# Kernel optimization log

Hardware: AMD Instinct MI355X
Metric: run time of the kernel (lower is better)

## Reference

```python
import jax, jax.numpy as jnp
import numpy as np

ENC_DIM = 512
B, T = 2048, 256
NUM_PARTS, PART_DIM, ATT_DIM, VOCAB = 64, 32, 128, 12


def _p(key, shape, scale=0.05):
    return jax.random.normal(key, shape, dtype=jnp.float32) * scale


def setup_inputs() -> dict:
    key = jax.random.key(0)
    ks = jax.random.split(key, 24)
    inp = {
        "img_features": jax.random.normal(ks[0], (B, 32, 8, 8), dtype=jnp.float32),
        "label": jax.random.normal(ks[1], (B, T, VOCAB), dtype=jnp.float32),
        # Attention params
        "Ww": _p(ks[2], (ATT_DIM, PART_DIM)), "Wb": _p(ks[3], (ATT_DIM,)),
        "Uw": _p(ks[4], (ATT_DIM, ENC_DIM)), "Ub": _p(ks[5], (ATT_DIM,)),
        "vw": _p(ks[6], (1, ATT_DIM)), "vb": _p(ks[7], (1,)),
        "betaw": _p(ks[8], (PART_DIM, ENC_DIM)), "betab": _p(ks[9], (PART_DIM,)),
        # init hidden params
        "ihw": _p(ks[10], (ENC_DIM, NUM_PARTS)), "ihb": _p(ks[11], (ENC_DIM,)),
        "icw": _p(ks[12], (ENC_DIM, NUM_PARTS)), "icb": _p(ks[13], (ENC_DIM,)),
        # LSTMCell params (PyTorch layout: [4*H, in] / [4*H, H])
        "W_ih": _p(ks[14], (4 * ENC_DIM, VOCAB + PART_DIM)),
        "W_hh": _p(ks[15], (4 * ENC_DIM, ENC_DIM)),
        "b_ih": _p(ks[16], (4 * ENC_DIM,)), "b_hh": _p(ks[17], (4 * ENC_DIM,)),
        # output fc
        "ow": _p(ks[18], (VOCAB, ENC_DIM)), "ob": _p(ks[19], (VOCAB,)),
    }
    return inp


def reference(img_features, label, Ww, Wb, Uw, Ub, vw, vb, betaw, betab,
              ihw, ihb, icw, icb, W_ih, W_hh, b_ih, b_hh, ow, ob):
    b = img_features.shape[0]
    feats = img_features.reshape(b, 32, -1)          # [B, 32, 64]
    parts = feats.transpose(0, 2, 1)                  # [B, 64, 32]
    # init hidden/cell from mean over channel dim (dim=1 in torch)
    avg = feats.mean(axis=1)                          # [B, 64]
    h0 = jnp.tanh(avg @ ihw.T + ihb)                  # [B, H]
    c0 = jnp.tanh(avg @ icw.T + icb)
    # W_s depends only on img features: hoist out of the loop (same math)
    Ws = parts @ Ww.T + Wb                            # [B, 64, 128]
    lab = label.transpose(1, 0, 2)                    # [T, B, 12]

    H = h0.shape[1]

    def step(carry, x_t):
        h, c = carry
        Uh = h @ Uw.T + Ub                            # [B, 128]
        att = jnp.tanh(Ws + Uh[:, None, :])           # [B, 64, 128]
        score = (att @ vw.T + vb)[..., 0]             # [B, 64]
        alpha = jax.nn.softmax(score, axis=1)
        ctx = jnp.einsum('bp,bpd->bd', alpha, parts)  # [B, 32]
        beta = jax.nn.sigmoid(h @ betaw.T + betab)
        ctx = ctx * beta
        inp = jnp.concatenate([x_t, ctx], axis=1)     # [B, 44]
        gates = inp @ W_ih.T + b_ih + h @ W_hh.T + b_hh
        i, f, g, o = jnp.split(gates, 4, axis=1)
        c2 = jax.nn.sigmoid(f) * c + jax.nn.sigmoid(i) * jnp.tanh(g)
        h2 = jax.nn.sigmoid(o) * jnp.tanh(c2)
        out = h2 @ ow.T + ob                          # [B, 12]
        return (h2, c2), (out, alpha)

    (_, _), (outs, alphas) = jax.lax.scan(step, (h0, c0), lab)
    output = jax.nn.log_softmax(outs, axis=-1).transpose(1, 0, 2)  # [B, T, 12]
    return output, alphas  # alphas: [T, B, 64] (stacked version of the list)
```

## Files before the change

kernel.cpp:

```cpp
#include <hip/hip_runtime.h>
#include <hip/hip_bf16.h>


typedef __attribute__((ext_vector_type(8))) short short8;
typedef __attribute__((ext_vector_type(4))) float floatx4;
typedef __attribute__((ext_vector_type(2))) unsigned int uint2v;

#define DEV static __device__ __forceinline__
#define C2LE 2.885390082f
#define LOG2E 1.4426950409f
#define LN2 0.6931471806f

DEV unsigned short f2bf(float f) {
    unsigned int u = __float_as_uint(f);
    unsigned int r = (u + 0x7FFFu + ((u >> 16) & 1u)) >> 16;
    return (unsigned short)r;
}
DEV float bf2f(unsigned short u) { return __uint_as_float(((unsigned int)u) << 16); }
DEV float rcp_f(float x) { float r; asm("v_rcp_f32 %0, %1" : "=v"(r) : "v"(x)); return r; }
DEV float tanh_f(float x) { return 1.f - 2.f * rcp_f(1.f + exp2f(x * C2LE)); }
DEV float sigm(float x) { return rcp_f(1.f + exp2f(-x * LOG2E)); }

DEV void ldg16_sc(short8* d, const unsigned short* p) {
    asm volatile("global_load_dwordx4 %0, %1, off sc0 sc1" : "=v"(*d) : "v"(p));
}
DEV void stg16_sc(unsigned short* p, short8 v) {
    asm volatile("global_store_dwordx4 %0, %1, off sc0 sc1" :: "v"(p), "v"(v) : "memory");
}
DEV void stg8_sc(unsigned short* p, uint2v v) {
    asm volatile("global_store_dwordx2 %0, %1, off sc0 sc1" :: "v"(p), "v"(v) : "memory");
}
DEV void st_flag(int* p, int v) {
    asm volatile("global_store_dword %0, %1, off sc0 sc1" :: "v"(p), "v"(v) : "memory");
}
DEV int ld_flag(const int* p) {
    int v;
    asm volatile("global_load_dword %0, %1, off sc0 sc1\n\ts_waitcnt vmcnt(0)"
                 : "=v"(v) : "v"(p) : "memory");
    return v;
}
DEV void waitv0() { asm volatile("s_waitcnt vmcnt(0)" ::: "memory"); }

#define OFF_XH     ((size_t)0)
#define OFF_C0     ((size_t)2359296)
#define OFF_PARTS  ((size_t)6553600)
#define OFF_WBIG   ((size_t)14942208)
#define OFF_WSMALL ((size_t)17301504)
#define OFF_WW2    ((size_t)17465344)
#define OFF_BIAS   ((size_t)17473536)
#define OFF_AVG    ((size_t)17481728)
#define OFF_FLAGS  ((size_t)18006016)

DEV void gbar(int* flags, int bk, int g4, int step) {
    waitv0();
    __syncthreads();
    if (threadIdx.x < 64) {
        int lane = threadIdx.x;
        if (lane == 0) st_flag(flags + bk * 32, step);
        for (;;) {
            int v = step;
            if (lane < 4) v = ld_flag(flags + (g4 + lane) * 32);
            if (__all(v >= step)) break;
            __builtin_amdgcn_s_sleep(1);
        }
    }
    __syncthreads();
}

__global__ void k_init(int* flags) {
    int i = blockIdx.x * 256 + threadIdx.x;
    if (i < 256 * 32) flags[i] = 0;
}

__global__ void k_avg(const float* __restrict__ img, float* __restrict__ avg) {
    int idx = blockIdx.x * 256 + threadIdx.x;
    int b = idx >> 6, p = idx & 63;
    const float* base = img + (size_t)b * 2048 + p;
    float s = 0.f;
#pragma unroll
    for (int k = 0; k < 32; ++k) s += base[k * 64];
    avg[idx] = s * (1.f / 32.f);
}

__global__ void k_prep(const float* __restrict__ Whh, const float* __restrict__ Wih,
                       const float* __restrict__ Uw, const float* __restrict__ betaw,
                       const float* __restrict__ Ww, const float* __restrict__ bih,
                       const float* __restrict__ bhh,
                       unsigned short* __restrict__ Wbig, unsigned short* __restrict__ Wsmall,
                       unsigned short* __restrict__ Ww2, float* __restrict__ bias_cat) {
    int p = blockIdx.x, tid = threadIdx.x;
    int g = p & 3, j = p >> 2, orig = g * 512 + j;
    for (int k = tid; k < 576; k += 256) {
        float v = 0.f;
        if (k < 512) v = Whh[(size_t)orig * 512 + k];
        else if (k < 556) v = Wih[(size_t)orig * 44 + (k - 512)];
        Wbig[(size_t)p * 576 + k] = f2bf(v);
    }
    if (p < 160) {
        for (int k = tid; k < 512; k += 256) {
            float v = (p < 128) ? Uw[(size_t)p * 512 + k] : betaw[(size_t)(p - 128) * 512 + k];
            Wsmall[(size_t)p * 512 + k] = f2bf(v);
        }
    }
    if (p < 128 && tid < 32) Ww2[p * 32 + tid] = f2bf(C2LE * Ww[p * 32 + tid]);
    if (tid == 0) bias_cat[orig] = bih[orig] + bhh[orig];
}

__global__ __launch_bounds__(512) void k_h0c0(const float* __restrict__ avg,
                                              const float* __restrict__ ihw, const float* __restrict__ ihb,
                                              const float* __restrict__ icw, const float* __restrict__ icb,
                                              unsigned short* __restrict__ xh, float* __restrict__ c0) {
    __shared__ float avg_s[8][64];
    int b0 = blockIdx.x * 8, tid = threadIdx.x;
    for (int i = tid; i < 8 * 64; i += 512) avg_s[i >> 6][i & 63] = avg[b0 * 64 + i];
    __syncthreads();
    int j = tid;
    float w0[64];
#pragma unroll
    for (int p4 = 0; p4 < 16; ++p4) {
        float4 v = ((const float4*)(ihw + j * 64))[p4];
        w0[p4 * 4 + 0] = v.x; w0[p4 * 4 + 1] = v.y; w0[p4 * 4 + 2] = v.z; w0[p4 * 4 + 3] = v.w;
    }
    float bh = ihb[j];
#pragma unroll
    for (int bb = 0; bb < 8; ++bb) {
        float s = bh;
#pragma unroll
        for (int p = 0; p < 64; ++p) s += w0[p] * avg_s[bb][p];
        xh[(size_t)(b0 + bb) * 576 + j] = f2bf(tanh_f(s));
        if (j < 20) xh[(size_t)(b0 + bb) * 576 + 556 + j] = 0;
    }
#pragma unroll
    for (int p4 = 0; p4 < 16; ++p4) {
        float4 v = ((const float4*)(icw + j * 64))[p4];
        w0[p4 * 4 + 0] = v.x; w0[p4 * 4 + 1] = v.y; w0[p4 * 4 + 2] = v.z; w0[p4 * 4 + 3] = v.w;
    }
    float bc = icb[j];
#pragma unroll
    for (int bb = 0; bb < 8; ++bb) {
        float s = bc;
#pragma unroll
        for (int p = 0; p < 64; ++p) s += w0[p] * avg_s[bb][p];
        c0[(size_t)(b0 + bb) * 512 + j] = tanh_f(s);
    }
}

__global__ __launch_bounds__(256) void k_parts(const float* __restrict__ img,
                                               unsigned short* __restrict__ parts_bf) {
    __shared__ float pl[64][33];
    int b = blockIdx.x, tid = threadIdx.x;
    const float* ib = img + (size_t)b * 2048;
    for (int i = tid; i < 2048; i += 256) pl[i & 63][i >> 6] = ib[i];
    __syncthreads();
    for (int i = tid; i < 2048; i += 256)
        parts_bf[(size_t)b * 2048 + i] = f2bf(pl[i >> 5][i & 31]);
}

__global__ __launch_bounds__(512, 2) void k_scan(
    unsigned short* __restrict__ xh,
    const float* __restrict__ c0,
    const unsigned short* __restrict__ parts_bf,
    const unsigned short* __restrict__ Wsmall, const unsigned short* __restrict__ Wbig,
    const unsigned short* __restrict__ Ww2, const float* __restrict__ bias_cat,
    const float* __restrict__ Ub, const float* __restrict__ betab, const float* __restrict__ Wb,
    const float* __restrict__ vw,
    const float* __restrict__ label, const float* __restrict__ ow, const float* __restrict__ ob,
    float* __restrict__ out_alpha, float* __restrict__ out_logits,
    int* __restrict__ flags)
{
    __shared__ unsigned short Ald[32 * 584];
    __shared__ unsigned short parts_l[8][2304];
    __shared__ unsigned short ow_l[12][512];
    __shared__ unsigned short h2scr[32][128];
    __shared__ float uh_l[8][160];
    __shared__ float al_l[8][64];
    __shared__ float bias_l[512];
    __shared__ unsigned short xscr[8][48];
    __shared__ float vw2_l[128];
    __shared__ float obl[12];

    const int tid = threadIdx.x, w = tid >> 6, lane = tid & 63;
    const int bk = blockIdx.x;
    const int mtile = bk >> 2, ntile = bk & 3;
    const int g4 = bk & ~3;
    const int wm = w >> 2, wn = w & 3;

    if (tid < 128) vw2_l[tid] = -2.f * vw[tid];
    if (tid < 12) obl[tid] = ob[tid];
    {
        int g = tid >> 7, jl = tid & 127;
        bias_l[tid] = bias_cat[g * 512 + ntile * 128 + jl];
    }
    for (int i = tid; i < 12 * 512; i += 512) ow_l[i >> 9][i & 511] = f2bf(ow[i]);
    {
        int row = tid >> 6, p = tid & 63;
        const short8* src = (const short8*)(parts_bf + (size_t)(bk * 8 + row) * 2048 + p * 32);
        short8* dst = (short8*)&parts_l[row][p * 36];
        dst[0] = src[0]; dst[1] = src[1]; dst[2] = src[2]; dst[3] = src[3];
    }
    float creg[32];
#pragma unroll
    for (int nf = 0; nf < 8; ++nf)
#pragma unroll
        for (int r = 0; r < 4; ++r) {
            int b = mtile * 32 + wm * 16 + (lane >> 4) * 4 + r;
            int j = ntile * 128 + wn * 32 + nf * 4 + (lane & 3);
            creg[nf * 4 + r] = c0[(size_t)b * 512 + j];
        }

    floatx4 acc[8];
    float vwsum = 0.f;

    auto stage32 = [&]() {
        short8 tv[4];
#pragma unroll
        for (int q = 0; q < 4; ++q) {
            int cid = tid + q * 512;
            int row = cid >> 6, c16 = cid & 63;
            ldg16_sc(&tv[q], xh + (size_t)(mtile * 32 + row) * 576 + c16 * 8);
        }
        waitv0();
        __builtin_amdgcn_sched_barrier(0);
#pragma unroll
        for (int q = 0; q < 4; ++q) {
            int cid = tid + q * 512;
            int row = cid >> 6, c16 = cid & 63;
            *(short8*)&Ald[row * 584 + c16 * 8] = tv[q];
        }
    };
    auto stage_tail = [&]() {
        if (tid < 256) {
            short8 tv;
            int row = tid >> 3, c16 = tid & 7;
            ldg16_sc(&tv, xh + (size_t)(mtile * 32 + row) * 576 + 512 + c16 * 8);
            waitv0();
            __builtin_amdgcn_sched_barrier(0);
            *(short8*)&Ald[row * 584 + 512 + c16 * 8] = tv;
        }
    };

    auto do_uh = [&]() {
        if (w < 5) {
            const unsigned short* Bp = Wsmall + (size_t)(w * 32 + (lane & 15)) * 512 + (lane >> 4) * 8;
            const unsigned short* Ab = &Ald[(ntile * 8 + (lane & 7)) * 584 + (lane >> 4) * 8];
            floatx4 u0 = {}, u1 = {};
#pragma unroll 4
            for (int k0 = 0; k0 < 512; k0 += 32) {
                short8 a = *(const short8*)(Ab + k0);
                u0 = __builtin_amdgcn_mfma_f32_16x16x32_bf16(a, *(const short8*)(Bp + k0), u0, 0, 0, 0);
                u1 = __builtin_amdgcn_mfma_f32_16x16x32_bf16(a, *(const short8*)(Bp + 16 * 512 + k0), u1, 0, 0, 0);
            }
            int r0 = (lane >> 4) * 4, cc = lane & 15;
            if (r0 < 8) {
#pragma unroll
                for (int q = 0; q < 2; ++q) {
                    int n = w * 32 + q * 16 + cc;
#pragma unroll
                    for (int r = 0; r < 4; ++r) {
                        float val = (q ? u1[r] : u0[r]);
                        uh_l[r0 + r][n] = (n < 128) ? C2LE * (val + Ub[n] + Wb[n])
                                                    : (val + betab[n - 128]);
                    }
                }
            }
        }
    };

    auto do_head = [&](int tt) {
        int b = bk * 8 + w;
        short8 hv = *(const short8*)&Ald[(ntile * 8 + w) * 584 + lane * 8];
        float hf[8];
#pragma unroll
        for (int j = 0; j < 8; ++j) hf[j] = bf2f((unsigned short)hv[j]);
        float ov[12];
#pragma unroll
        for (int v = 0; v < 12; ++v) {
            short8 wv = *(const short8*)&ow_l[v][lane * 8];
            float p = 0.f;
#pragma unroll
            for (int j = 0; j < 8; ++j) p += hf[j] * bf2f((unsigned short)wv[j]);
#pragma unroll
            for (int o = 32; o; o >>= 1) p += __shfl_xor(p, o);
            ov[v] = p + obl[v];
        }
        float mx = ov[0];
#pragma unroll
        for (int v = 1; v < 12; ++v) mx = fmaxf(mx, ov[v]);
        float ss = 0.f;
#pragma unroll
        for (int v = 0; v < 12; ++v) ss += exp2f((ov[v] - mx) * LOG2E);
        float lse = mx + log2f(ss) * LN2;
#pragma unroll
        for (int v = 0; v < 12; ++v)
            if (lane == v) out_logits[((size_t)b * 256 + tt) * 12 + v] = ov[v] - lse;
    };

    auto do_attn = [&](int tt) {
        int b = bk * 8 + w;
        short8 pa[4];
#pragma unroll
        for (int mt = 0; mt < 4; ++mt)
            pa[mt] = *(const short8*)&parts_l[w][(mt * 16 + (lane & 15)) * 36 + (lane >> 4) * 8];
        float sc[4][4] = {};
#pragma unroll
        for (int nt = 0; nt < 8; ++nt) {
            short8 wwf = *(const short8*)(Ww2 + (size_t)((lane & 15) + 16 * nt) * 32 + (lane >> 4) * 8);
            int d = nt * 16 + (lane & 15);
            float ud = uh_l[w][d];
            float v2 = vw2_l[d];
#pragma unroll
            for (int mt = 0; mt < 4; ++mt) {
                floatx4 z = {};
                floatx4 wsa = __builtin_amdgcn_mfma_f32_16x16x32_bf16(pa[mt], wwf, z, 0, 0, 0);
#pragma unroll
                for (int r = 0; r < 4; ++r)
                    sc[mt][r] += v2 * rcp_f(1.f + exp2f(wsa[r] + ud));
            }
        }
        float mx = -1e30f;
#pragma unroll
        for (int mt = 0; mt < 4; ++mt)
#pragma unroll
            for (int r = 0; r < 4; ++r) {
                float s = sc[mt][r];
                s += __shfl_xor(s, 1); s += __shfl_xor(s, 2);
                s += __shfl_xor(s, 4); s += __shfl_xor(s, 8);
                s += vwsum;
                sc[mt][r] = s;
                mx = fmaxf(mx, s);
            }
        mx = fmaxf(mx, __shfl_xor(mx, 16));
        mx = fmaxf(mx, __shfl_xor(mx, 32));
        float ssum = 0.f;
        float av[4][4];
#pragma unroll
        for (int mt = 0; mt < 4; ++mt)
#pragma unroll
            for (int r = 0; r < 4; ++r) {
                av[mt][r] = exp2f((sc[mt][r] - mx) * LOG2E);
                ssum += av[mt][r];
            }
        ssum += __shfl_xor(ssum, 16);
        ssum += __shfl_xor(ssum, 32);
        float rs = rcp_f(ssum);
#pragma unroll
        for (int mt = 0; mt < 4; ++mt) {
            if ((lane & 15) == mt) {
                float4 fv = make_float4(av[mt][0] * rs, av[mt][1] * rs, av[mt][2] * rs, av[mt][3] * rs);
                int p0 = mt * 16 + (lane >> 4) * 4;
                *(float4*)&out_alpha[((size_t)tt * 2048 + b) * 64 + p0] = fv;
                *(float4*)&al_l[w][p0] = fv;
            }
        }
        int k = lane & 31, half = lane >> 5;
        float cp = 0.f;
#pragma unroll
        for (int p = 0; p < 32; ++p) {
            int pp = half * 32 + p;
            cp += al_l[w][pp] * bf2f(parts_l[w][pp * 36 + k]);
        }
        cp += __shfl_xor(cp, 32);
        if (half == 0) xscr[w][12 + k] = f2bf(cp * sigm(uh_l[w][128 + k]));
        if (lane < 12) xscr[w][lane] = f2bf(label[((size_t)b * 256 + tt) * 12 + lane]);
        if (lane < 11) {
            uint2v v = *(const uint2v*)&xscr[w][lane * 4];
            stg8_sc(xh + (size_t)b * 576 + 512 + lane * 4, v);
        }
    };

    auto gemm_h = [&]() {
        const unsigned short* Bp = Wbig + (size_t)(ntile * 512 + wn * 128 + (lane & 15)) * 576 + (lane >> 4) * 8;
        const unsigned short* Ab = &Ald[(wm * 16 + (lane & 15)) * 584 + (lane >> 4) * 8];
#pragma unroll
        for (int nf = 0; nf < 8; ++nf) acc[nf] = (floatx4){0.f, 0.f, 0.f, 0.f};
#pragma unroll 2
        for (int kk = 0; kk < 16; ++kk) {
            int k0 = kk * 32;
            short8 a = *(const short8*)(Ab + k0);
#pragma unroll
            for (int nf = 0; nf < 8; ++nf) {
                short8 bv = *(const short8*)(Bp + (size_t)nf * 9216 + k0);
                acc[nf] = __builtin_amdgcn_mfma_f32_16x16x32_bf16(a, bv, acc[nf], 0, 0, 0);
            }
        }
    };
    auto gemm_tail_cell = [&]() {
        const unsigned short* Bp = Wbig + (size_t)(ntile * 512 + wn * 128 + (lane & 15)) * 576 + (lane >> 4) * 8;
        const unsigned short* Ab = &Ald[(wm * 16 + (lane & 15)) * 584 + (lane >> 4) * 8];
#pragma unroll
        for (int kk = 16; kk < 18; ++kk) {
            int k0 = kk * 32;
            short8 a = *(const short8*)(Ab + k0);
#pragma unroll
            for (int nf = 0; nf < 8; ++nf) {
                short8 bv = *(const short8*)(Bp + (size_t)nf * 9216 + k0);
                acc[nf] = __builtin_amdgcn_mfma_f32_16x16x32_bf16(a, bv, acc[nf], 0, 0, 0);
            }
        }
        int base = (lane & 48) | ((lane & 3) * 4);
#pragma unroll
        for (int nf = 0; nf < 8; ++nf) {
            int jl = wn * 32 + nf * 4 + (lane & 3);
            float bi = bias_l[jl], bfv = bias_l[128 + jl], bg = bias_l[256 + jl], bo = bias_l[384 + jl];
#pragma unroll
            for (int r = 0; r < 4; ++r) {
                float x = acc[nf][r];
                float g0 = __shfl(x, base + 0);
                float g1 = __shfl(x, base + 1);
                float g2 = __shfl(x, base + 2);
                float g3 = __shfl(x, base + 3);
                int ci = nf * 4 + r;
                float c2 = sigm(g1 + bfv) * creg[ci] + sigm(g0 + bi) * tanh_f(g2 + bg);
                creg[ci] = c2;
                float h2 = sigm(g3 + bo) * tanh_f(c2);
                if (((lane >> 2) & 3) == 0) {
                    int row = wm * 16 + (lane >> 4) * 4 + r;
                    h2scr[row][wn * 32 + nf * 4 + (lane & 3)] = f2bf(h2);
                }
            }
        }
        __syncthreads();
        {
            int row = tid >> 4, seg = tid & 15;
            short8 v = *(const short8*)&h2scr[row][seg * 8];
            stg16_sc(xh + (size_t)(mtile * 32 + row) * 576 + ntile * 128 + seg * 8, v);
        }
    };

    stage32();
    __syncthreads();
    {
        float s = 0.f;
#pragma unroll
        for (int d = 0; d < 128; ++d) s += vw2_l[d];
        vwsum = -0.5f * s;
    }
    do_uh();
    __syncthreads();
    do_attn(0);

    int bc = 0;
    for (int t = 0; t < 256; ++t) {
        gemm_h();
        gbar(flags, bk, g4, ++bc);
        stage_tail();
        __syncthreads();
        gemm_tail_cell();
        gbar(flags, bk, g4, ++bc);
        stage32();
        __syncthreads();
        do_head(t);
        if (t < 255) {
            do_uh();
            __syncthreads();
            do_attn(t + 1);
        }
    }
}

extern "C" void kernel_launch(void* const* d_in, const int* in_sizes, int n_in,
                              void* d_out, int out_size, void* d_ws, size_t ws_size,
                              hipStream_t stream) {
    const float* img   = (const float*)d_in[0];
    const float* label = (const float*)d_in[1];
    const float* Ww    = (const float*)d_in[2];
    const float* Wb    = (const float*)d_in[3];
    const float* Uw    = (const float*)d_in[4];
    const float* Ub    = (const float*)d_in[5];
    const float* vw    = (const float*)d_in[6];
    const float* betaw = (const float*)d_in[8];
    const float* betab = (const float*)d_in[9];
    const float* ihw   = (const float*)d_in[10];
    const float* ihb   = (const float*)d_in[11];
    const float* icw   = (const float*)d_in[12];
    const float* icb   = (const float*)d_in[13];
    const float* Wih   = (const float*)d_in[14];
    const float* Whh   = (const float*)d_in[15];
    const float* bih   = (const float*)d_in[16];
    const float* bhh   = (const float*)d_in[17];
    const float* ow    = (const float*)d_in[18];
    const float* ob    = (const float*)d_in[19];

    char* ws = (char*)d_ws;
    unsigned short* xh       = (unsigned short*)(ws + OFF_XH);
    float*          c0       = (float*)(ws + OFF_C0);
    unsigned short* parts_bf = (unsigned short*)(ws + OFF_PARTS);
    unsigned short* Wbig     = (unsigned short*)(ws + OFF_WBIG);
    unsigned short* Wsmall   = (unsigned short*)(ws + OFF_WSMALL);
    unsigned short* Ww2      = (unsigned short*)(ws + OFF_WW2);
    float*          bias     = (float*)(ws + OFF_BIAS);
    float*          avg      = (float*)(ws + OFF_AVG);
    int*            flags    = (int*)(ws + OFF_FLAGS);

    float* out_logits = (float*)d_out;
    float* out_alpha  = out_logits + (size_t)2048 * 256 * 12;

    k_init<<<32, 256, 0, stream>>>(flags);
    k_avg<<<512, 256, 0, stream>>>(img, avg);
    k_prep<<<2048, 256, 0, stream>>>(Whh, Wih, Uw, betaw, Ww, bih, bhh, Wbig, Wsmall, Ww2, bias);
    k_h0c0<<<256, 512, 0, stream>>>(avg, ihw, ihb, icw, icb, xh, c0);
    k_parts<<<2048, 256, 0, stream>>>(img, parts_bf);

    k_scan<<<256, 512, 0, stream>>>(xh, c0, parts_bf, Wsmall, Wbig, Ww2, bias,
                                    Ub, betab, Wb, vw, label, ow, ob,
                                    out_alpha, out_logits, flags);
}
```

Measured before the change: 14.27 ms.

## Split persistent scan into 512 blocks of 16 batch rows with 4 waves

The persistent LSTM scan kernel now launches 512 blocks of 256 threads, each owning 16 batch rows instead of 32, with the per-step work (U·h GEMM, attention, cell GEMM) remapped onto 4 waves. Parts data is no longer staged in LDS and is read directly from global memory during attention, and the attention bias is folded into the MFMA accumulator initial value. The intent is to spread the serial recurrence across more CUs with smaller per-block LDS. In exchange there are more blocks in the flag-based barriers, each block reloads its Wbig weight slice with half the row reuse, and parts are re-read from global or cache every step.

```diff
diff --git a/kernel.cpp b/kernel.cpp
--- a/kernel.cpp
+++ b/kernel.cpp
@@ -69,7 +69,7 @@
 
 __global__ void k_init(int* flags) {
     int i = blockIdx.x * 256 + threadIdx.x;
-    if (i < 256 * 32) flags[i] = 0;
+    if (i < 512 * 32) flags[i] = 0;
 }
 
 __global__ void k_avg(const float* __restrict__ img, float* __restrict__ avg) {
@@ -156,7 +156,7 @@
         parts_bf[(size_t)b * 2048 + i] = f2bf(pl[i >> 5][i & 31]);
 }
 
-__global__ __launch_bounds__(512, 2) void k_scan(
+__global__ __launch_bounds__(256, 2) void k_scan(
     unsigned short* __restrict__ xh,
     const float* __restrict__ c0,
     const unsigned short* __restrict__ parts_bf,
@@ -168,14 +168,13 @@
     float* __restrict__ out_alpha, float* __restrict__ out_logits,
     int* __restrict__ flags)
 {
-    __shared__ unsigned short Ald[32 * 584];
-    __shared__ unsigned short parts_l[8][2304];
+    __shared__ unsigned short Ald[16 * 584];
     __shared__ unsigned short ow_l[12][512];
-    __shared__ unsigned short h2scr[32][128];
-    __shared__ float uh_l[8][160];
-    __shared__ float al_l[8][64];
+    __shared__ unsigned short h2scr[16][128];
+    __shared__ float uh_l[16][160];
+    __shared__ float al_l[4][64];
     __shared__ float bias_l[512];
-    __shared__ unsigned short xscr[8][48];
+    __shared__ unsigned short xscr[4][48];
     __shared__ float vw2_l[128];
     __shared__ float obl[12];
 
@@ -183,56 +182,53 @@
     const int bk = blockIdx.x;
     const int mtile = bk >> 2, ntile = bk & 3;
     const int g4 = bk & ~3;
-    const int wm = w >> 2, wn = w & 3;
 
     if (tid < 128) vw2_l[tid] = -2.f * vw[tid];
     if (tid < 12) obl[tid] = ob[tid];
-    {
-        int g = tid >> 7, jl = tid & 127;
-        bias_l[tid] = bias_cat[g * 512 + ntile * 128 + jl];
-    }
-    for (int i = tid; i < 12 * 512; i += 512) ow_l[i >> 9][i & 511] = f2bf(ow[i]);
-    {
-        int row = tid >> 6, p = tid & 63;
-        const short8* src = (const short8*)(parts_bf + (size_t)(bk * 8 + row) * 2048 + p * 32);
-        short8* dst = (short8*)&parts_l[row][p * 36];
-        dst[0] = src[0]; dst[1] = src[1]; dst[2] = src[2]; dst[3] = src[3];
+    for (int i = tid; i < 512; i += 256) {
+        int g = i >> 7, jl = i & 127;
+        bias_l[i] = bias_cat[g * 512 + ntile * 128 + jl];
+    }
+    for (int i = tid; i < 12 * 512; i += 256) ow_l[i >> 9][i & 511] = f2bf(ow[i]);
+    for (int i = tid; i < 16 * 20; i += 256) {
+        int row = i / 20, cc = 556 + (i % 20);
+        Ald[row * 584 + cc] = 0;
     }
     float creg[32];
 #pragma unroll
     for (int nf = 0; nf < 8; ++nf)
 #pragma unroll
         for (int r = 0; r < 4; ++r) {
-            int b = mtile * 32 + wm * 16 + (lane >> 4) * 4 + r;
-            int j = ntile * 128 + wn * 32 + nf * 4 + (lane & 3);
+            int b = mtile * 16 + (lane >> 4) * 4 + r;
+            int j = ntile * 128 + w * 32 + nf * 4 + (lane & 3);
             creg[nf * 4 + r] = c0[(size_t)b * 512 + j];
         }
 
     floatx4 acc[8];
     float vwsum = 0.f;
 
-    auto stage32 = [&]() {
+    auto stage16 = [&]() {
         short8 tv[4];
 #pragma unroll
         for (int q = 0; q < 4; ++q) {
-            int cid = tid + q * 512;
+            int cid = tid + q * 256;
             int row = cid >> 6, c16 = cid & 63;
-            ldg16_sc(&tv[q], xh + (size_t)(mtile * 32 + row) * 576 + c16 * 8);
+            ldg16_sc(&tv[q], xh + (size_t)(mtile * 16 + row) * 576 + c16 * 8);
         }
         waitv0();
         __builtin_amdgcn_sched_barrier(0);
 #pragma unroll
         for (int q = 0; q < 4; ++q) {
-            int cid = tid + q * 512;
+            int cid = tid + q * 256;
             int row = cid >> 6, c16 = cid & 63;
             *(short8*)&Ald[row * 584 + c16 * 8] = tv[q];
         }
     };
     auto stage_tail = [&]() {
-        if (tid < 256) {
+        if (tid < 128) {
             short8 tv;
             int row = tid >> 3, c16 = tid & 7;
-            ldg16_sc(&tv, xh + (size_t)(mtile * 32 + row) * 576 + 512 + c16 * 8);
+            ldg16_sc(&tv, xh + (size_t)(mtile * 16 + row) * 576 + 512 + c16 * 8);
             waitv0();
             __builtin_amdgcn_sched_barrier(0);
             *(short8*)&Ald[row * 584 + 512 + c16 * 8] = tv;
@@ -240,35 +236,27 @@
     };
 
     auto do_uh = [&]() {
-        if (w < 5) {
-            const unsigned short* Bp = Wsmall + (size_t)(w * 32 + (lane & 15)) * 512 + (lane >> 4) * 8;
-            const unsigned short* Ab = &Ald[(ntile * 8 + (lane & 7)) * 584 + (lane >> 4) * 8];
-            floatx4 u0 = {}, u1 = {};
+        for (int nt = w; nt < 10; nt += 4) {
+            const unsigned short* Bp = Wsmall + (size_t)(nt * 16 + (lane & 15)) * 512 + (lane >> 4) * 8;
+            const unsigned short* Ab = &Ald[(lane & 15) * 584 + (lane >> 4) * 8];
+            floatx4 u = {};
 #pragma unroll 4
             for (int k0 = 0; k0 < 512; k0 += 32) {
                 short8 a = *(const short8*)(Ab + k0);
-                u0 = __builtin_amdgcn_mfma_f32_16x16x32_bf16(a, *(const short8*)(Bp + k0), u0, 0, 0, 0);
-                u1 = __builtin_amdgcn_mfma_f32_16x16x32_bf16(a, *(const short8*)(Bp + 16 * 512 + k0), u1, 0, 0, 0);
-            }
-            int r0 = (lane >> 4) * 4, cc = lane & 15;
-            if (r0 < 8) {
-#pragma unroll
-                for (int q = 0; q < 2; ++q) {
-                    int n = w * 32 + q * 16 + cc;
-#pragma unroll
-                    for (int r = 0; r < 4; ++r) {
-                        float val = (q ? u1[r] : u0[r]);
-                        uh_l[r0 + r][n] = (n < 128) ? C2LE * (val + Ub[n] + Wb[n])
-                                                    : (val + betab[n - 128]);
-                    }
-                }
-            }
+                u = __builtin_amdgcn_mfma_f32_16x16x32_bf16(a, *(const short8*)(Bp + k0), u, 0, 0, 0);
+            }
+            int n = nt * 16 + (lane & 15), r0 = (lane >> 4) * 4;
+            float addv = (n < 128) ? (Ub[n] + Wb[n]) : betab[n - 128];
+            float scl = (n < 128) ? C2LE : 1.f;
+#pragma unroll
+            for (int r = 0; r < 4; ++r) uh_l[r0 + r][n] = (u[r] + addv) * scl;
         }
     };
 
     auto do_head = [&](int tt) {
-        int b = bk * 8 + w;
-        short8 hv = *(const short8*)&Ald[(ntile * 8 + w) * 584 + lane * 8];
+        int lr = ntile * 4 + w;
+        int b = bk * 4 + w;
+        short8 hv = *(const short8*)&Ald[lr * 584 + lane * 8];
         float hf[8];
 #pragma unroll
         for (int j = 0; j < 8; ++j) hf[j] = bf2f((unsigned short)hv[j]);
@@ -296,25 +284,27 @@
     };
 
     auto do_attn = [&](int tt) {
-        int b = bk * 8 + w;
+        int lr = ntile * 4 + w;
+        int b = bk * 4 + w;
+        const unsigned short* pb = parts_bf + (size_t)b * 2048;
         short8 pa[4];
 #pragma unroll
         for (int mt = 0; mt < 4; ++mt)
-            pa[mt] = *(const short8*)&parts_l[w][(mt * 16 + (lane & 15)) * 36 + (lane >> 4) * 8];
+            pa[mt] = *(const short8*)(pb + ((lane & 15) + 16 * mt) * 32 + (lane >> 4) * 8);
         float sc[4][4] = {};
 #pragma unroll
         for (int nt = 0; nt < 8; ++nt) {
             short8 wwf = *(const short8*)(Ww2 + (size_t)((lane & 15) + 16 * nt) * 32 + (lane >> 4) * 8);
             int d = nt * 16 + (lane & 15);
-            float ud = uh_l[w][d];
+            float ud = uh_l[lr][d];
             float v2 = vw2_l[d];
+            floatx4 ini = {ud, ud, ud, ud};
 #pragma unroll
             for (int mt = 0; mt < 4; ++mt) {
-                floatx4 z = {};
-                floatx4 wsa = __builtin_amdgcn_mfma_f32_16x16x32_bf16(pa[mt], wwf, z, 0, 0, 0);
+                floatx4 wsa = __builtin_amdgcn_mfma_f32_16x16x32_bf16(pa[mt], wwf, ini, 0, 0, 0);
 #pragma unroll
                 for (int r = 0; r < 4; ++r)
-                    sc[mt][r] += v2 * rcp_f(1.f + exp2f(wsa[r] + ud));
+                    sc[mt][r] += v2 * rcp_f(1.f + exp2f(wsa[r]));
             }
         }
         float mx = -1e30f;
@@ -357,10 +347,10 @@
 #pragma unroll
         for (int p = 0; p < 32; ++p) {
             int pp = half * 32 + p;
-            cp += al_l[w][pp] * bf2f(parts_l[w][pp * 36 + k]);
+            cp += al_l[w][pp] * bf2f(pb[pp * 32 + k]);
         }
         cp += __shfl_xor(cp, 32);
-        if (half == 0) xscr[w][12 + k] = f2bf(cp * sigm(uh_l[w][128 + k]));
+        if (half == 0) xscr[w][12 + k] = f2bf(cp * sigm(uh_l[lr][128 + k]));
         if (lane < 12) xscr[w][lane] = f2bf(label[((size_t)b * 256 + tt) * 12 + lane]);
         if (lane < 11) {
             uint2v v = *(const uint2v*)&xscr[w][lane * 4];
@@ -369,8 +359,8 @@
     };
 
     auto gemm_h = [&]() {
-        const unsigned short* Bp = Wbig + (size_t)(ntile * 512 + wn * 128 + (lane & 15)) * 576 + (lane >> 4) * 8;
-        const unsigned short* Ab = &Ald[(wm * 16 + (lane & 15)) * 584 + (lane >> 4) * 8];
+        const unsigned short* Bp = Wbig + (size_t)(ntile * 512 + w * 128 + (lane & 15)) * 576 + (lane >> 4) * 8;
+        const unsigned short* Ab = &Ald[(lane & 15) * 584 + (lane >> 4) * 8];
 #pragma unroll
         for (int nf = 0; nf < 8; ++nf) acc[nf] = (floatx4){0.f, 0.f, 0.f, 0.f};
 #pragma unroll 2
@@ -385,8 +375,8 @@
         }
     };
     auto gemm_tail_cell = [&]() {
-        const unsigned short* Bp = Wbig + (size_t)(ntile * 512 + wn * 128 + (lane & 15)) * 576 + (lane >> 4) * 8;
-        const unsigned short* Ab = &Ald[(wm * 16 + (lane & 15)) * 584 + (lane >> 4) * 8];
+        const unsigned short* Bp = Wbig + (size_t)(ntile * 512 + w * 128 + (lane & 15)) * 576 + (lane >> 4) * 8;
+        const unsigned short* Ab = &Ald[(lane & 15) * 584 + (lane >> 4) * 8];
 #pragma unroll
         for (int kk = 16; kk < 18; ++kk) {
             int k0 = kk * 32;
@@ -400,7 +390,7 @@
         int base = (lane & 48) | ((lane & 3) * 4);
 #pragma unroll
         for (int nf = 0; nf < 8; ++nf) {
-            int jl = wn * 32 + nf * 4 + (lane & 3);
+            int jl = w * 32 + nf * 4 + (lane & 3);
             float bi = bias_l[jl], bfv = bias_l[128 + jl], bg = bias_l[256 + jl], bo = bias_l[384 + jl];
 #pragma unroll
             for (int r = 0; r < 4; ++r) {
@@ -414,8 +404,8 @@
                 creg[ci] = c2;
                 float h2 = sigm(g3 + bo) * tanh_f(c2);
                 if (((lane >> 2) & 3) == 0) {
-                    int row = wm * 16 + (lane >> 4) * 4 + r;
-                    h2scr[row][wn * 32 + nf * 4 + (lane & 3)] = f2bf(h2);
+                    int row = (lane >> 4) * 4 + r;
+                    h2scr[row][jl] = f2bf(h2);
                 }
             }
         }
@@ -423,11 +413,11 @@
         {
             int row = tid >> 4, seg = tid & 15;
             short8 v = *(const short8*)&h2scr[row][seg * 8];
-            stg16_sc(xh + (size_t)(mtile * 32 + row) * 576 + ntile * 128 + seg * 8, v);
-        }
-    };
-
-    stage32();
+            stg16_sc(xh + (size_t)(mtile * 16 + row) * 576 + ntile * 128 + seg * 8, v);
+        }
+    };
+
+    stage16();
     __syncthreads();
     {
         float s = 0.f;
@@ -447,7 +437,7 @@
         __syncthreads();
         gemm_tail_cell();
         gbar(flags, bk, g4, ++bc);
-        stage32();
+        stage16();
         __syncthreads();
         do_head(t);
         if (t < 255) {
@@ -495,13 +485,13 @@
     float* out_logits = (float*)d_out;
     float* out_alpha  = out_logits + (size_t)2048 * 256 * 12;
 
-    k_init<<<32, 256, 0, stream>>>(flags);
+    k_init<<<64, 256, 0, stream>>>(flags);
     k_avg<<<512, 256, 0, stream>>>(img, avg);
     k_prep<<<2048, 256, 0, stream>>>(Whh, Wih, Uw, betaw, Ww, bih, bhh, Wbig, Wsmall, Ww2, bias);
     k_h0c0<<<256, 512, 0, stream>>>(avg, ihw, ihb, icw, icb, xh, c0);
     k_parts<<<2048, 256, 0, stream>>>(img, parts_bf);
 
-    k_scan<<<256, 512, 0, stream>>>(xh, c0, parts_bf, Wsmall, Wbig, Ww2, bias,
+    k_scan<<<512, 256, 0, stream>>>(xh, c0, parts_bf, Wsmall, Wbig, Ww2, bias,
                                     Ub, betab, Wb, vw, label, ow, ob,
                                     out_alpha, out_logits, flags);
 }
```

Measured after the change: 14.30 ms. About the same (+0.2%).
